# Kernel optimization log

Measured on AMD Instinct MI355X. Metric: run time of the kernel, lower is better.

Reference implementation:

```python
import jax, jax.numpy as jnp
import numpy as np

NV, NE, D, NNZ = 100000, 50000, 128, 1600000
EPS = 1e-5

def _seg_mean(vals, idx, n):
    # vals: [nnz, d] gathered rows; mean-aggregate into n segments
    s = jax.ops.segment_sum(vals, idx, num_segments=n)
    c = jax.ops.segment_sum(jnp.ones((idx.shape[0], 1), vals.dtype), idx, num_segments=n)
    return s / jnp.maximum(c, 1.0)

def _linear(x, W, b):
    return x @ W.T + b

def _layer_norm(x, g, b):
    m = jnp.mean(x, axis=-1, keepdims=True)
    v = jnp.mean((x - m) ** 2, axis=-1, keepdims=True)
    return (x - m) * jax.lax.rsqrt(v + EPS) * g + b

def setup_inputs() -> dict:
    key = jax.random.key(0)
    ks = jax.random.split(key, 12)
    inp = {
        "X": jax.random.normal(ks[0], (NV, D), jnp.float32),
        "Y": jax.random.normal(ks[1], (NE, D), jnp.float32),
        "v_idx": jax.random.randint(ks[2], (NNZ,), 0, NV, jnp.int32),
        "e_idx": jax.random.randint(ks[3], (NNZ,), 0, NE, jnp.int32),
        "W_tv": jax.random.normal(ks[4], (D, D), jnp.float32) * 0.05,
        "b_tv": jnp.zeros((D,), jnp.float32),
        "W_te": jax.random.normal(ks[5], (D, D), jnp.float32) * 0.05,
        "b_te": jnp.zeros((D,), jnp.float32),
        "W_em": jax.random.normal(ks[6], (D, 2 * D), jnp.float32) * 0.05,
        "b_em": jnp.zeros((D,), jnp.float32),
        "W_vm": jax.random.normal(ks[7], (D, 2 * D), jnp.float32) * 0.05,
        "b_vm": jnp.zeros((D,), jnp.float32),
        "g_v": jnp.ones((D,), jnp.float32),
        "be_v": jnp.zeros((D,), jnp.float32),
        "g_e": jnp.ones((D,), jnp.float32),
        "be_e": jnp.zeros((D,), jnp.float32),
    }
    return inp

def reference(X, Y, v_idx, e_idx, W_tv, b_tv, W_te, b_te, W_em, b_em, W_vm, b_vm, g_v, be_v, g_e, be_e):
    X0, Y0 = X, Y
    Xp = _linear(X0, W_tv, b_tv)                       # [NV, D] theta_vertex
    # v2e aggregation (mean): gather vertex rows per incidence, reduce to edges
    msg_e = _seg_mean(Xp[v_idx], e_idx, NE)            # [NE, D]
    Ym = _linear(jnp.concatenate([Y0, msg_e], axis=-1), W_em, b_em)  # edge_merge
    Ym = _linear(Ym, W_te, b_te)                       # theta_edge
    # e2v aggregation (mean)
    msg_v = _seg_mean(Ym[e_idx], v_idx, NV)            # [NV, D]
    Xm = _linear(jnp.concatenate([X0, msg_v], axis=-1), W_vm, b_vm)  # vertex_merge
    Xo = jax.nn.relu(_layer_norm(Xm, g_v, be_v))       # dropout is identity at eval / p=0
    Yo = jax.nn.relu(_layer_norm(Ym, g_e, be_e))
    return (Xo, Yo)
```

## Files before the change

### kernel.cpp

```cpp
#include <hip/hip_runtime.h>
#include <stdint.h>

#define NVERT 100000
#define NEDGE 50000
#define DIM 128
#define NNZ_N 1600000
#define N4 (NNZ_N / 4)
#define CAP_E 96
#define NB_CNT 1563
#define NB_G1 1563
#define NB_SEG1 3125
#define NB_WV 1563

typedef __attribute__((ext_vector_type(8))) short bf16x8;
typedef __attribute__((ext_vector_type(4))) float f32x4;

__device__ __forceinline__ unsigned short f32_to_bf16(float f) {
  union { float f; unsigned u; } v; v.f = f;
  unsigned r = v.u + 0x7fffu + ((v.u >> 16) & 1u);
  return (unsigned short)(r >> 16);
}
__device__ __forceinline__ float bf16_lo(unsigned u) {
  union { unsigned u; float f; } v; v.u = u << 16; return v.f;
}
__device__ __forceinline__ float bf16_hi(unsigned u) {
  union { unsigned u; float f; } v; v.u = u & 0xffff0000u; return v.f;
}
__device__ __forceinline__ float ldf(const void* p, long i, int bf) {
  if (bf) {
    union { unsigned u; float f; } v;
    v.u = (unsigned)((const unsigned short*)p)[i] << 16;
    return v.f;
  }
  return ((const float*)p)[i];
}
__device__ __forceinline__ bf16x8 frag_ext(const void* A, long idx, int bf) {
  if (bf) return *(const bf16x8*)((const unsigned short*)A + idx);
  const float* f = (const float*)A + idx;
  float4 f0 = *(const float4*)f, f1 = *(const float4*)(f + 4);
  bf16x8 r;
  r[0] = (short)f32_to_bf16(f0.x); r[1] = (short)f32_to_bf16(f0.y);
  r[2] = (short)f32_to_bf16(f0.z); r[3] = (short)f32_to_bf16(f0.w);
  r[4] = (short)f32_to_bf16(f1.x); r[5] = (short)f32_to_bf16(f1.y);
  r[6] = (short)f32_to_bf16(f1.z); r[7] = (short)f32_to_bf16(f1.w);
  return r;
}
__device__ __forceinline__ bf16x8 frag_f32(const float* f) {
  float4 f0 = *(const float4*)f, f1 = *(const float4*)(f + 4);
  bf16x8 r;
  r[0] = (short)f32_to_bf16(f0.x); r[1] = (short)f32_to_bf16(f0.y);
  r[2] = (short)f32_to_bf16(f0.z); r[3] = (short)f32_to_bf16(f0.w);
  r[4] = (short)f32_to_bf16(f1.x); r[5] = (short)f32_to_bf16(f1.y);
  r[6] = (short)f32_to_bf16(f1.z); r[7] = (short)f32_to_bf16(f1.w);
  return r;
}

__device__ __forceinline__ int block_flag(const unsigned short* x) {
  __shared__ int cnt;
  if (threadIdx.x == 0) cnt = 0;
  __syncthreads();
  int c = 0;
#pragma unroll
  for (int k = 0; k < 4; ++k) {
    unsigned short h = x[(threadIdx.x * 4 + k) * 2];
    int ex = (h >> 7) & 0xFF;
    c += (ex >= 100 && ex <= 140) ? 1 : 0;
  }
  atomicAdd(&cnt, c);
  __syncthreads();
  return cnt > 512;
}

__global__ __launch_bounds__(256) void prep_all(
    const unsigned short* __restrict__ Xu,
    const void* __restrict__ btv, const void* __restrict__ bvm,
    const void* __restrict__ Wtv, const void* __restrict__ Wvm,
    const void* __restrict__ Wte, const void* __restrict__ Wem,
    const void* __restrict__ bte, const void* __restrict__ bem,
    float* __restrict__ btvf, float* __restrict__ bvmf, float* __restrict__ bcf,
    unsigned short* __restrict__ Wtvb, unsigned short* __restrict__ Wvmb,
    unsigned short* __restrict__ Wcb, int* __restrict__ flag) {
  int bf = block_flag(Xu);
  int b = blockIdx.x, t = threadIdx.x;
  if (b == 0) {
    if (t == 0) flag[0] = bf;
    if (t < 128) btvf[t] = ldf(btv, t, bf);
    else bvmf[t - 128] = ldf(bvm, t - 128, bf);
  } else if (b < 65) {
    int i = (b - 1) * 256 + t;
    Wtvb[i] = f32_to_bf16(ldf(Wtv, i, bf));
  } else if (b < 193) {
    int i = (b - 65) * 256 + t;
    Wvmb[i] = f32_to_bf16(ldf(Wvm, i, bf));
  } else {
    int n = b - 193, k = t;
    float acc = 0.f;
    for (int j = 0; j < 128; ++j)
      acc += ldf(Wte, n * 128 + j, bf) * ldf(Wem, j * 256 + k, bf);
    Wcb[n * 256 + k] = f32_to_bf16(acc);
    if (k == 0) {
      float bb = ldf(bte, n, bf);
      for (int j = 0; j < 128; ++j) bb += ldf(Wte, n * 128 + j, bf) * ldf(bem, j, bf);
      bcf[n] = bb;
    }
  }
}

__device__ __forceinline__ void count_body(
    const int4* __restrict__ vi, const int4* __restrict__ ei,
    int* __restrict__ cnt_v, int* __restrict__ cnt_e,
    int* __restrict__ adj_e, int4* __restrict__ tV, int bid) {
  int i = bid * 256 + threadIdx.x;
  if (i >= N4) return;
  int4 e = ei[i], v = vi[i];
  int t;
  t = atomicAdd(&cnt_e[e.x], 1); if (t < CAP_E) adj_e[e.x * CAP_E + t] = v.x;
  t = atomicAdd(&cnt_e[e.y], 1); if (t < CAP_E) adj_e[e.y * CAP_E + t] = v.y;
  t = atomicAdd(&cnt_e[e.z], 1); if (t < CAP_E) adj_e[e.z * CAP_E + t] = v.z;
  t = atomicAdd(&cnt_e[e.w], 1); if (t < CAP_E) adj_e[e.w * CAP_E + t] = v.w;
  int4 tv;
  tv.x = atomicAdd(&cnt_v[v.x], 1);
  tv.y = atomicAdd(&cnt_v[v.y], 1);
  tv.z = atomicAdd(&cnt_v[v.z], 1);
  tv.w = atomicAdd(&cnt_v[v.w], 1);
  tV[i] = tv;
}

__device__ __forceinline__ void wadjv_body(
    const int4* __restrict__ vi, const int4* __restrict__ ei,
    const int4* __restrict__ tV, const int* __restrict__ off_v,
    int* __restrict__ adj_v, int bid) {
  int i = bid * 256 + threadIdx.x;
  if (i >= N4) return;
  int4 e = ei[i], v = vi[i], tv = tV[i];
  adj_v[off_v[v.x] + tv.x] = e.x;
  adj_v[off_v[v.y] + tv.y] = e.y;
  adj_v[off_v[v.z] + tv.z] = e.z;
  adj_v[off_v[v.w] + tv.w] = e.w;
}

__global__ __launch_bounds__(1024) void scan_block(const int* __restrict__ in,
                                                   int* __restrict__ out,
                                                   int* __restrict__ bsum, int n) {
  __shared__ int sd[1024];
  const int tid = threadIdx.x;
  const int i = blockIdx.x * 1024 + tid;
  int x = (i < n) ? in[i] : 0;
  sd[tid] = x;
  __syncthreads();
  int v = x;
  for (int s = 1; s < 1024; s <<= 1) {
    int t = (tid >= s) ? sd[tid - s] : 0;
    __syncthreads();
    v += t;
    sd[tid] = v;
    __syncthreads();
  }
  if (i < n) out[i] = v - x;
  if (tid == 1023) bsum[blockIdx.x] = v;
}

__global__ __launch_bounds__(1024) void scan_sums(int* __restrict__ bsum, int nb) {
  __shared__ int sd[1024];
  const int tid = threadIdx.x;
  int x = (tid < nb) ? bsum[tid] : 0;
  sd[tid] = x;
  __syncthreads();
  int v = x;
  for (int s = 1; s < 1024; s <<= 1) {
    int t = (tid >= s) ? sd[tid - s] : 0;
    __syncthreads();
    v += t;
    sd[tid] = v;
    __syncthreads();
  }
  if (tid < nb) bsum[tid] = v - x;
}

__global__ void scan_add(int* __restrict__ out, const int* __restrict__ bsum, int n, int total) {
  int i = blockIdx.x * blockDim.x + threadIdx.x;
  if (i < n) out[i] += bsum[i >> 10];
  if (i == 0) out[n] = total;
}

template<bool CAPMODE>
__device__ __forceinline__ void seg_body(
    const int* __restrict__ off_or_cnt, const int* __restrict__ adj,
    const unsigned short* __restrict__ tbl, float* __restrict__ out,
    int nseg, int nrows, int bid) {
  const int seg = (bid * 256 + threadIdx.x) >> 4;
  const int l = threadIdx.x & 15;
  if (seg >= nseg) return;
  int s, e, cnt;
  if (CAPMODE) {
    cnt = off_or_cnt[seg];
    s = seg * CAP_E;
    e = s + (cnt < CAP_E ? cnt : CAP_E);
  } else {
    s = off_or_cnt[seg];
    e = off_or_cnt[seg + 1];
    cnt = e - s;
  }
  float a0 = 0, a1 = 0, a2 = 0, a3 = 0, a4 = 0, a5 = 0, a6 = 0, a7 = 0;
#define ACC(u)                                         \
  a0 += bf16_lo(u.x); a1 += bf16_hi(u.x);              \
  a2 += bf16_lo(u.y); a3 += bf16_hi(u.y);              \
  a4 += bf16_lo(u.z); a5 += bf16_hi(u.z);              \
  a6 += bf16_lo(u.w); a7 += bf16_hi(u.w);
  int i = s;
  for (; i + 4 <= e; i += 4) {
    int r0 = adj[i], r1 = adj[i + 1], r2 = adj[i + 2], r3 = adj[i + 3];
    if ((unsigned)r0 >= (unsigned)nrows) r0 = 0;
    if ((unsigned)r1 >= (unsigned)nrows) r1 = 0;
    if ((unsigned)r2 >= (unsigned)nrows) r2 = 0;
    if ((unsigned)r3 >= (unsigned)nrows) r3 = 0;
    uint4 u0 = *(const uint4*)(tbl + (long)r0 * DIM + l * 8);
    uint4 u1 = *(const uint4*)(tbl + (long)r1 * DIM + l * 8);
    uint4 u2 = *(const uint4*)(tbl + (long)r2 * DIM + l * 8);
    uint4 u3 = *(const uint4*)(tbl + (long)r3 * DIM + l * 8);
    ACC(u0) ACC(u1) ACC(u2) ACC(u3)
  }
  for (; i < e; ++i) {
    int r = adj[i];
    if ((unsigned)r >= (unsigned)nrows) r = 0;
    uint4 u = *(const uint4*)(tbl + (long)r * DIM + l * 8);
    ACC(u)
  }
#undef ACC
  float inv = (cnt > 0) ? 1.f / (float)cnt : 0.f;
  float* op = out + (long)seg * DIM + l * 8;
  *(float4*)op       = make_float4(a0 * inv, a1 * inv, a2 * inv, a3 * inv);
  *(float4*)(op + 4) = make_float4(a4 * inv, a5 * inv, a6 * inv, a7 * inv);
}

template<int KSTEPS, bool SPLIT, bool DO_LN, bool STORE_BF16>
__device__ __forceinline__ void gemm_body(
    int bid,
    const void* __restrict__ A0, const float* __restrict__ A1,
    const unsigned short* __restrict__ Bw, const float* __restrict__ biasf,
    unsigned short* __restrict__ outb, float* __restrict__ outf,
    const void* __restrict__ gw_, const void* __restrict__ bw_,
    int M, const int* flagp) {
  constexpr int K = KSTEPS * 32;
  constexpr int KA0 = SPLIT ? 128 : K;
  const int bf = *flagp;
  const int wave = threadIdx.x >> 6;
  const int lane = threadIdx.x & 63;
  const int m0 = bid * 64 + wave * 16;
  if (m0 >= M) return;
  const int c = lane & 15;
  const int q = lane >> 4;
  const long arow = m0 + c;

  f32x4 acc[8];
#pragma unroll
  for (int t = 0; t < 8; ++t) acc[t] = (f32x4){0.f, 0.f, 0.f, 0.f};

#pragma unroll
  for (int ks = 0; ks < KSTEPS; ++ks) {
    const int kk = ks * 32 + q * 8;
    bf16x8 a;
    if (SPLIT && ks >= KSTEPS / 2) a = frag_f32(A1 + arow * 128 + (kk - 128));
    else                           a = frag_ext(A0, arow * (long)KA0 + kk, bf);
#pragma unroll
    for (int t = 0; t < 8; ++t) {
      bf16x8 b = *(const bf16x8*)(Bw + (long)(t * 16 + c) * K + kk);
      acc[t] = __builtin_amdgcn_mfma_f32_16x16x32_bf16(a, b, acc[t], 0, 0, 0);
    }
  }

#pragma unroll
  for (int t = 0; t < 8; ++t) {
    float bv = biasf[t * 16 + c];
#pragma unroll
    for (int i = 0; i < 4; ++i) acc[t][i] += bv;
  }

  if (STORE_BF16) {
#pragma unroll
    for (int t = 0; t < 8; ++t) {
      int col = t * 16 + c;
#pragma unroll
      for (int i = 0; i < 4; ++i)
        outb[(long)(m0 + q * 4 + i) * DIM + col] = f32_to_bf16(acc[t][i]);
    }
  }

  if (DO_LN) {
    float sum[4] = {0, 0, 0, 0}, sq[4] = {0, 0, 0, 0};
#pragma unroll
    for (int t = 0; t < 8; ++t)
#pragma unroll
      for (int i = 0; i < 4; ++i) { float v = acc[t][i]; sum[i] += v; sq[i] += v * v; }
#pragma unroll
    for (int m = 1; m <= 8; m <<= 1) {
#pragma unroll
      for (int i = 0; i < 4; ++i) {
        sum[i] += __shfl_xor(sum[i], m, 64);
        sq[i]  += __shfl_xor(sq[i], m, 64);
      }
    }
    float mean[4], rstd[4];
#pragma unroll
    for (int i = 0; i < 4; ++i) {
      mean[i] = sum[i] * (1.0f / 128.0f);
      float var = sq[i] * (1.0f / 128.0f) - mean[i] * mean[i];
      rstd[i] = rsqrtf(var + 1e-5f);
    }
#pragma unroll
    for (int t = 0; t < 8; ++t) {
      int col = t * 16 + c;
      float gv = ldf(gw_, col, bf), bv = ldf(bw_, col, bf);
#pragma unroll
      for (int i = 0; i < 4; ++i) {
        float v = (acc[t][i] - mean[i]) * rstd[i] * gv + bv;
        v = v > 0.f ? v : 0.f;
        outf[(long)(m0 + q * 4 + i) * DIM + col] = v;
      }
    }
  }
}

__global__ __launch_bounds__(256) void k_count_gemm1(
    const int4* __restrict__ vi, const int4* __restrict__ ei,
    int* __restrict__ cnt_v, int* __restrict__ cnt_e,
    int* __restrict__ adj_e, int4* __restrict__ tV,
    const void* __restrict__ X, const unsigned short* __restrict__ Wtvb,
    const float* __restrict__ btvf, unsigned short* __restrict__ Xp_b,
    const int* __restrict__ flagp) {
  if (blockIdx.x & 1)
    gemm_body<4, false, false, true>(blockIdx.x >> 1, X, nullptr, Wtvb, btvf,
                                     Xp_b, nullptr, nullptr, nullptr, NVERT, flagp);
  else
    count_body(vi, ei, cnt_v, cnt_e, adj_e, tV, blockIdx.x >> 1);
}

__global__ __launch_bounds__(256) void k_seg1_wadjv(
    const int* __restrict__ cnt_e, const int* __restrict__ adj_e,
    const unsigned short* __restrict__ Xp_b, float* __restrict__ msg_e,
    const int4* __restrict__ vi, const int4* __restrict__ ei,
    const int4* __restrict__ tV, const int* __restrict__ off_v,
    int* __restrict__ adj_v) {
  int r = blockIdx.x % 3, q = blockIdx.x / 3;
  if (r == 2)
    wadjv_body(vi, ei, tV, off_v, adj_v, q);
  else
    seg_body<true>(cnt_e, adj_e, Xp_b, msg_e, NEDGE, NVERT, q * 2 + r);
}

__global__ __launch_bounds__(256) void seg_mean_off(
    const int* __restrict__ off, const int* __restrict__ adj,
    const unsigned short* __restrict__ tbl, float* __restrict__ out,
    int nseg, int nrows) {
  seg_body<false>(off, adj, tbl, out, nseg, nrows, blockIdx.x);
}

template<int KSTEPS, bool SPLIT, bool DO_LN, bool STORE_BF16>
__global__ __launch_bounds__(256) void gemm_mfma(
    const void* __restrict__ A0, const float* __restrict__ A1,
    const unsigned short* __restrict__ Bw, const float* __restrict__ biasf,
    unsigned short* __restrict__ outb, float* __restrict__ outf,
    const void* __restrict__ gw_, const void* __restrict__ bw_,
    int M, const int* flagp) {
  gemm_body<KSTEPS, SPLIT, DO_LN, STORE_BF16>(blockIdx.x, A0, A1, Bw, biasf,
                                              outb, outf, gw_, bw_, M, flagp);
}

extern "C" void kernel_launch(void* const* d_in, const int* in_sizes, int n_in,
                              void* d_out, int out_size, void* d_ws, size_t ws_size,
                              hipStream_t stream) {
  const void* X    = d_in[0];
  const void* Y    = d_in[1];
  const int*  v_idx = (const int*)d_in[2];
  const int*  e_idx = (const int*)d_in[3];
  const void* W_tv = d_in[4];
  const void* b_tv = d_in[5];
  const void* W_te = d_in[6];
  const void* b_te = d_in[7];
  const void* W_em = d_in[8];
  const void* b_em = d_in[9];
  const void* W_vm = d_in[10];
  const void* b_vm = d_in[11];
  const void* g_v  = d_in[12];
  const void* be_v = d_in[13];
  const void* g_e  = d_in[14];
  const void* be_e = d_in[15];

  unsigned short* Xp_b = (unsigned short*)d_out;
  int*   adj_e = (int*)((char*)d_out + 25600000);
  int4*  tV4   = (int4*)((char*)d_out + 44800000);
  float* msg_e = (float*)d_out + (long)NVERT * DIM;
  float* Yo    = msg_e;
  float* msg_v = (float*)d_out;
  float* Xo    = (float*)d_out;

  char* p = (char*)d_ws;
  auto alloc = [&](size_t n) { char* r = p; p += (n + 255) & ~(size_t)255; return r; };
  int*   flag  = (int*)alloc(4);
  float* btv_f = (float*)alloc(DIM * 4);
  float* bvm_f = (float*)alloc(DIM * 4);
  float* bc_f  = (float*)alloc(DIM * 4);
  unsigned short* Wtv_b = (unsigned short*)alloc(DIM * DIM * 2);
  unsigned short* Wvm_b = (unsigned short*)alloc(2 * DIM * DIM * 2);
  unsigned short* Wc_b  = (unsigned short*)alloc(2 * DIM * DIM * 2);
  unsigned short* Ym_b  = (unsigned short*)alloc((long)NEDGE * DIM * 2);
  int* off_v  = (int*)alloc((NVERT + 1) * 4);
  int* cnt_e  = (int*)alloc(NEDGE * 4);
  int* cnt_v  = (int*)alloc(NVERT * 4);
  int* bsum_v = (int*)alloc(((NVERT + 1023) / 1024) * 4);
  int* adj_v  = (int*)alloc((long)NNZ_N * 4);

  prep_all<<<321, 256, 0, stream>>>(
      (const unsigned short*)X, b_tv, b_vm, W_tv, W_vm, W_te, W_em, b_te, b_em,
      btv_f, bvm_f, bc_f, Wtv_b, Wvm_b, Wc_b, flag);

  hipMemsetAsync(cnt_e, 0, NEDGE * 4, stream);
  hipMemsetAsync(cnt_v, 0, NVERT * 4, stream);
  k_count_gemm1<<<NB_CNT + NB_G1, 256, 0, stream>>>(
      (const int4*)v_idx, (const int4*)e_idx, cnt_v, cnt_e, adj_e, tV4,
      X, Wtv_b, btv_f, Xp_b, flag);

  {
    int nbv = (NVERT + 1023) / 1024;
    scan_block<<<nbv, 1024, 0, stream>>>(cnt_v, off_v, bsum_v, NVERT);
    scan_sums<<<1, 1024, 0, stream>>>(bsum_v, nbv);
    scan_add<<<(NVERT + 255) / 256, 256, 0, stream>>>(off_v, bsum_v, NVERT, NNZ_N);
  }

  k_seg1_wadjv<<<3 * NB_WV, 256, 0, stream>>>(
      cnt_e, adj_e, Xp_b, msg_e,
      (const int4*)v_idx, (const int4*)e_idx, tV4, off_v, adj_v);

  gemm_mfma<8, true, true, true><<<(NEDGE + 63) / 64, 256, 0, stream>>>(
      Y, msg_e, Wc_b, bc_f, Ym_b, Yo, g_e, be_e, NEDGE, flag);

  seg_mean_off<<<(NVERT + 15) / 16, 256, 0, stream>>>(
      off_v, adj_v, Ym_b, msg_v, NVERT, NEDGE);

  gemm_mfma<8, true, true, false><<<(NVERT + 63) / 64, 256, 0, stream>>>(
      X, msg_v, Wvm_b, bvm_f, nullptr, Xo, g_v, be_v, NVERT, flag);
}
```

Measured before the change: 576.7 us.

## Regroup graph-build stages into fewer fused launches and drop the scan-add pass

Zeroing of the edge and vertex counters moves into extra blocks of the prep kernel, replacing two memsets. Edge and vertex counting are split: edge counting stays fused with the first GEMM, and vertex counting now runs alongside the first segment-mean. The scan_add pass is removed; consumers add the per-block scan sum when they read offsets. The vertex adjacency scatter is fused with the edge-merge GEMM in one launch. The aim is fewer launches and serialization points and more overlap between independent stages, at the cost of extra bsum lookups in the scatter and segment kernels and more complex block-role dispatch.

```diff
diff --git a/kernel.cpp b/kernel.cpp
--- a/kernel.cpp
+++ b/kernel.cpp
@@ -7,10 +7,7 @@
 #define NNZ_N 1600000
 #define N4 (NNZ_N / 4)
 #define CAP_E 96
-#define NB_CNT 1563
-#define NB_G1 1563
-#define NB_SEG1 3125
-#define NB_WV 1563
+#define NB_QTR 1563
 
 typedef __attribute__((ext_vector_type(8))) short bf16x8;
 typedef __attribute__((ext_vector_type(4))) float f32x4;
@@ -79,9 +76,16 @@
     const void* __restrict__ bte, const void* __restrict__ bem,
     float* __restrict__ btvf, float* __restrict__ bvmf, float* __restrict__ bcf,
     unsigned short* __restrict__ Wtvb, unsigned short* __restrict__ Wvmb,
-    unsigned short* __restrict__ Wcb, int* __restrict__ flag) {
+    unsigned short* __restrict__ Wcb, int* __restrict__ flag,
+    int* __restrict__ cnt_e, int* __restrict__ cnt_v) {
+  int b = blockIdx.x, t = threadIdx.x;
+  if (b >= 321) {
+    int i = (b - 321) * 256 + t;
+    if (i < NEDGE) cnt_e[i] = 0;
+    else if (i < NEDGE + NVERT) cnt_v[i - NEDGE] = 0;
+    return;
+  }
   int bf = block_flag(Xu);
-  int b = blockIdx.x, t = threadIdx.x;
   if (b == 0) {
     if (t == 0) flag[0] = bf;
     if (t < 128) btvf[t] = ldf(btv, t, bf);
@@ -106,10 +110,9 @@
   }
 }
 
-__device__ __forceinline__ void count_body(
+__device__ __forceinline__ void ecount_body(
     const int4* __restrict__ vi, const int4* __restrict__ ei,
-    int* __restrict__ cnt_v, int* __restrict__ cnt_e,
-    int* __restrict__ adj_e, int4* __restrict__ tV, int bid) {
+    int* __restrict__ cnt_e, int* __restrict__ adj_e, int bid) {
   int i = bid * 256 + threadIdx.x;
   if (i >= N4) return;
   int4 e = ei[i], v = vi[i];
@@ -118,6 +121,14 @@
   t = atomicAdd(&cnt_e[e.y], 1); if (t < CAP_E) adj_e[e.y * CAP_E + t] = v.y;
   t = atomicAdd(&cnt_e[e.z], 1); if (t < CAP_E) adj_e[e.z * CAP_E + t] = v.z;
   t = atomicAdd(&cnt_e[e.w], 1); if (t < CAP_E) adj_e[e.w * CAP_E + t] = v.w;
+}
+
+__device__ __forceinline__ void vcount_body(
+    const int4* __restrict__ vi, int* __restrict__ cnt_v,
+    int4* __restrict__ tV, int bid) {
+  int i = bid * 256 + threadIdx.x;
+  if (i >= N4) return;
+  int4 v = vi[i];
   int4 tv;
   tv.x = atomicAdd(&cnt_v[v.x], 1);
   tv.y = atomicAdd(&cnt_v[v.y], 1);
@@ -129,14 +140,14 @@
 __device__ __forceinline__ void wadjv_body(
     const int4* __restrict__ vi, const int4* __restrict__ ei,
     const int4* __restrict__ tV, const int* __restrict__ off_v,
-    int* __restrict__ adj_v, int bid) {
+    const int* __restrict__ bsum, int* __restrict__ adj_v, int bid) {
   int i = bid * 256 + threadIdx.x;
   if (i >= N4) return;
   int4 e = ei[i], v = vi[i], tv = tV[i];
-  adj_v[off_v[v.x] + tv.x] = e.x;
-  adj_v[off_v[v.y] + tv.y] = e.y;
-  adj_v[off_v[v.z] + tv.z] = e.z;
-  adj_v[off_v[v.w] + tv.w] = e.w;
+  adj_v[off_v[v.x] + bsum[v.x >> 10] + tv.x] = e.x;
+  adj_v[off_v[v.y] + bsum[v.y >> 10] + tv.y] = e.y;
+  adj_v[off_v[v.z] + bsum[v.z >> 10] + tv.z] = e.z;
+  adj_v[off_v[v.w] + bsum[v.w >> 10] + tv.w] = e.w;
 }
 
 __global__ __launch_bounds__(1024) void scan_block(const int* __restrict__ in,
@@ -177,17 +188,11 @@
   if (tid < nb) bsum[tid] = v - x;
 }
 
-__global__ void scan_add(int* __restrict__ out, const int* __restrict__ bsum, int n, int total) {
-  int i = blockIdx.x * blockDim.x + threadIdx.x;
-  if (i < n) out[i] += bsum[i >> 10];
-  if (i == 0) out[n] = total;
-}
-
 template<bool CAPMODE>
 __device__ __forceinline__ void seg_body(
     const int* __restrict__ off_or_cnt, const int* __restrict__ adj,
     const unsigned short* __restrict__ tbl, float* __restrict__ out,
-    int nseg, int nrows, int bid) {
+    int nseg, int nrows, const int* __restrict__ bsum, int total, int bid) {
   const int seg = (bid * 256 + threadIdx.x) >> 4;
   const int l = threadIdx.x & 15;
   if (seg >= nseg) return;
@@ -197,8 +202,8 @@
     s = seg * CAP_E;
     e = s + (cnt < CAP_E ? cnt : CAP_E);
   } else {
-    s = off_or_cnt[seg];
-    e = off_or_cnt[seg + 1];
+    s = off_or_cnt[seg] + bsum[seg >> 10];
+    e = (seg + 1 < nseg) ? off_or_cnt[seg + 1] + bsum[(seg + 1) >> 10] : total;
     cnt = e - s;
   }
   float a0 = 0, a1 = 0, a2 = 0, a3 = 0, a4 = 0, a5 = 0, a6 = 0, a7 = 0;
@@ -321,10 +326,9 @@
   }
 }
 
-__global__ __launch_bounds__(256) void k_count_gemm1(
+__global__ __launch_bounds__(256) void k_ecount_gemm1(
     const int4* __restrict__ vi, const int4* __restrict__ ei,
-    int* __restrict__ cnt_v, int* __restrict__ cnt_e,
-    int* __restrict__ adj_e, int4* __restrict__ tV,
+    int* __restrict__ cnt_e, int* __restrict__ adj_e,
     const void* __restrict__ X, const unsigned short* __restrict__ Wtvb,
     const float* __restrict__ btvf, unsigned short* __restrict__ Xp_b,
     const int* __restrict__ flagp) {
@@ -332,27 +336,44 @@
     gemm_body<4, false, false, true>(blockIdx.x >> 1, X, nullptr, Wtvb, btvf,
                                      Xp_b, nullptr, nullptr, nullptr, NVERT, flagp);
   else
-    count_body(vi, ei, cnt_v, cnt_e, adj_e, tV, blockIdx.x >> 1);
-}
-
-__global__ __launch_bounds__(256) void k_seg1_wadjv(
+    ecount_body(vi, ei, cnt_e, adj_e, blockIdx.x >> 1);
+}
+
+__global__ __launch_bounds__(256) void k_vcount_seg1(
+    const int4* __restrict__ vi, int* __restrict__ cnt_v, int4* __restrict__ tV,
     const int* __restrict__ cnt_e, const int* __restrict__ adj_e,
-    const unsigned short* __restrict__ Xp_b, float* __restrict__ msg_e,
+    const unsigned short* __restrict__ Xp_b, float* __restrict__ msg_e) {
+  int r = blockIdx.x % 3, q = blockIdx.x / 3;
+  if (r == 0)
+    vcount_body(vi, cnt_v, tV, q);
+  else
+    seg_body<true>(cnt_e, adj_e, Xp_b, msg_e, NEDGE, NVERT, nullptr, 0,
+                   q * 2 + (r - 1));
+}
+
+__global__ __launch_bounds__(256) void k_wadjv_gemm2(
     const int4* __restrict__ vi, const int4* __restrict__ ei,
     const int4* __restrict__ tV, const int* __restrict__ off_v,
-    int* __restrict__ adj_v) {
+    const int* __restrict__ bsum, int* __restrict__ adj_v,
+    const void* __restrict__ Y, const float* __restrict__ msg_e,
+    const unsigned short* __restrict__ Wcb, const float* __restrict__ bcf,
+    unsigned short* __restrict__ Ym_b, float* __restrict__ Yo,
+    const void* __restrict__ g_e, const void* __restrict__ be_e,
+    const int* __restrict__ flagp) {
   int r = blockIdx.x % 3, q = blockIdx.x / 3;
   if (r == 2)
-    wadjv_body(vi, ei, tV, off_v, adj_v, q);
+    gemm_body<8, true, true, true>(q, Y, msg_e, Wcb, bcf, Ym_b, Yo, g_e, be_e,
+                                   NEDGE, flagp);
   else
-    seg_body<true>(cnt_e, adj_e, Xp_b, msg_e, NEDGE, NVERT, q * 2 + r);
-}
-
-__global__ __launch_bounds__(256) void seg_mean_off(
-    const int* __restrict__ off, const int* __restrict__ adj,
-    const unsigned short* __restrict__ tbl, float* __restrict__ out,
-    int nseg, int nrows) {
-  seg_body<false>(off, adj, tbl, out, nseg, nrows, blockIdx.x);
+    wadjv_body(vi, ei, tV, off_v, bsum, adj_v, q * 2 + r);
+}
+
+__global__ __launch_bounds__(256) void seg_mean_v(
+    const int* __restrict__ off_v, const int* __restrict__ bsum,
+    const int* __restrict__ adj_v, const unsigned short* __restrict__ Ym_b,
+    float* __restrict__ msg_v) {
+  seg_body<false>(off_v, adj_v, Ym_b, msg_v, NVERT, NEDGE, bsum, NNZ_N,
+                  blockIdx.x);
 }
 
 template<int KSTEPS, bool SPLIT, bool DO_LN, bool STORE_BF16>
@@ -410,32 +431,29 @@
   int* bsum_v = (int*)alloc(((NVERT + 1023) / 1024) * 4);
   int* adj_v  = (int*)alloc((long)NNZ_N * 4);
 
-  prep_all<<<321, 256, 0, stream>>>(
+  prep_all<<<321 + (NEDGE + NVERT + 255) / 256, 256, 0, stream>>>(
       (const unsigned short*)X, b_tv, b_vm, W_tv, W_vm, W_te, W_em, b_te, b_em,
-      btv_f, bvm_f, bc_f, Wtv_b, Wvm_b, Wc_b, flag);
-
-  hipMemsetAsync(cnt_e, 0, NEDGE * 4, stream);
-  hipMemsetAsync(cnt_v, 0, NVERT * 4, stream);
-  k_count_gemm1<<<NB_CNT + NB_G1, 256, 0, stream>>>(
-      (const int4*)v_idx, (const int4*)e_idx, cnt_v, cnt_e, adj_e, tV4,
+      btv_f, bvm_f, bc_f, Wtv_b, Wvm_b, Wc_b, flag, cnt_e, cnt_v);
+
+  k_ecount_gemm1<<<2 * NB_QTR, 256, 0, stream>>>(
+      (const int4*)v_idx, (const int4*)e_idx, cnt_e, adj_e,
       X, Wtv_b, btv_f, Xp_b, flag);
+
+  k_vcount_seg1<<<3 * NB_QTR, 256, 0, stream>>>(
+      (const int4*)v_idx, cnt_v, tV4, cnt_e, adj_e, Xp_b, msg_e);
 
   {
     int nbv = (NVERT + 1023) / 1024;
     scan_block<<<nbv, 1024, 0, stream>>>(cnt_v, off_v, bsum_v, NVERT);
     scan_sums<<<1, 1024, 0, stream>>>(bsum_v, nbv);
-    scan_add<<<(NVERT + 255) / 256, 256, 0, stream>>>(off_v, bsum_v, NVERT, NNZ_N);
-  }
-
-  k_seg1_wadjv<<<3 * NB_WV, 256, 0, stream>>>(
-      cnt_e, adj_e, Xp_b, msg_e,
-      (const int4*)v_idx, (const int4*)e_idx, tV4, off_v, adj_v);
-
-  gemm_mfma<8, true, true, true><<<(NEDGE + 63) / 64, 256, 0, stream>>>(
-      Y, msg_e, Wc_b, bc_f, Ym_b, Yo, g_e, be_e, NEDGE, flag);
-
-  seg_mean_off<<<(NVERT + 15) / 16, 256, 0, stream>>>(
-      off_v, adj_v, Ym_b, msg_v, NVERT, NEDGE);
+  }
+
+  k_wadjv_gemm2<<<3 * ((NEDGE + 63) / 64), 256, 0, stream>>>(
+      (const int4*)v_idx, (const int4*)e_idx, tV4, off_v, bsum_v, adj_v,
+      Y, msg_e, Wc_b, bc_f, Ym_b, Yo, g_e, be_e, flag);
+
+  seg_mean_v<<<(NVERT + 15) / 16, 256, 0, stream>>>(
+      off_v, bsum_v, adj_v, Ym_b, msg_v);
 
   gemm_mfma<8, true, true, false><<<(NVERT + 63) / 64, 256, 0, stream>>>(
       X, msg_v, Wvm_b, bvm_f, nullptr, Xo, g_v, be_v, NVERT, flag);
```

Result: no change. 574.7 us (-0.3%).
